# Performance work log

Measured on AMD Instinct MI355X. Metric: run time of the kernel, lower is better.

## Reference

```python
import jax, jax.numpy as jnp
import numpy as np

EPS = 1e-5   # BatchNorm eps (eval mode, running_mean=0, running_var=1 as at init)
NEG = 0.2    # LeakyReLU negative slope


def _conv(W, x):
    # 1x1 conv == channel matmul. W: [out_c, in_c], x: [B, in_c, ...]
    return jnp.einsum('oc,bc...->bo...', W, x)


def _bn(x, g, b):
    # eval-mode BN with running_mean=0, running_var=1
    sh = (1, -1) + (1,) * (x.ndim - 2)
    return x * (g.reshape(sh) / np.float32(np.sqrt(1.0 + EPS))) + b.reshape(sh)


def _lrelu(x):
    return jax.nn.leaky_relu(x, NEG)


def _knn_idx(pos, k):
    # pos: [B, 3, N] -> idx [B, N, k] of k nearest points (incl. self)
    sq = jnp.sum(pos * pos, axis=1)                      # [B, N]
    inner = jnp.einsum('bcn,bcm->bnm', pos, pos)         # [B, N, N]
    dist = sq[:, :, None] + sq[:, None, :] - 2.0 * inner
    _, idx = jax.lax.top_k(-dist, k)
    return idx


def _gather(points, idx):
    # points [B, N, C], idx [B, N, K] -> [B, N, K, C]
    return jax.vmap(lambda p, i: p[i])(points, idx)


def setup_inputs() -> dict:
    key = jax.random.key(0)
    B, N, K = 2, 8192, 16
    d_points, d_model = 64, 64
    ks = jax.random.split(key, 24)
    w = lambda k_, o, i: (jax.random.normal(k_, (o, i), jnp.float32) * 0.05)
    gm = lambda k_, c: (1.0 + 0.1 * jax.random.normal(k_, (c,), jnp.float32))
    bt = lambda k_, c: (0.1 * jax.random.normal(k_, (c,), jnp.float32))
    return {
        'feats': jax.random.normal(ks[0], (B, d_points, N), jnp.float32),
        'pos': jax.random.uniform(ks[1], (B, 3, N), jnp.float32),
        'k': K,
        'W1': w(ks[2], d_model, d_points), 'g1': gm(ks[3], d_model), 'b1': bt(ks[4], d_model),
        'Wq': w(ks[5], d_model, d_model), 'Wk': w(ks[6], d_model, d_model), 'Wv': w(ks[7], d_model, d_model),
        'Wd1': w(ks[8], d_model, 3), 'gd1': gm(ks[9], d_model), 'bd1': bt(ks[10], d_model),
        'Wd2': w(ks[11], d_model, d_model), 'gd2': gm(ks[12], d_model), 'bd2': bt(ks[13], d_model),
        'Wg1': w(ks[14], d_model, d_model), 'gg1': gm(ks[15], d_model), 'bg1': bt(ks[16], d_model),
        'Wg2': w(ks[17], d_model, d_model), 'gg2': gm(ks[18], d_model), 'bg2': bt(ks[19], d_model),
        'W2': w(ks[20], d_points, d_model), 'g2': gm(ks[21], d_points), 'b2': bt(ks[22], d_points),
    }


def reference(feats, pos, k, W1, g1, b1, Wq, Wk, Wv,
              Wd1, gd1, bd1, Wd2, gd2, bd2,
              Wg1, gg1, bg1, Wg2, gg2, bg2, W2, g2, b2):
    B, _, N = feats.shape
    knn_idx = _knn_idx(pos, k)                            # [B, N, K]
    pos_nc = jnp.transpose(pos, (0, 2, 1))                # [B, N, 3]
    knn_pos = _gather(pos_nc, knn_idx)                    # [B, N, K, 3]

    x = _lrelu(_bn(_conv(W1, feats), g1, b1))             # [B, d, N]
    q = _conv(Wq, x)                                      # [B, d, N]
    k_feat = _gather(jnp.transpose(_conv(Wk, x), (0, 2, 1)), knn_idx)
    k_t = jnp.transpose(k_feat, (0, 3, 2, 1))             # [B, d, K, N]
    v_feat = _gather(jnp.transpose(_conv(Wv, x), (0, 2, 1)), knn_idx)
    v_t = jnp.transpose(v_feat, (0, 3, 2, 1))             # [B, d, K, N]

    rel = pos_nc[:, :, None, :] - knn_pos                 # [B, N, K, 3]
    rel_t = jnp.transpose(rel, (0, 3, 2, 1))              # [B, 3, K, N]
    pe = _lrelu(_bn(_conv(Wd1, rel_t), gd1, bd1))
    pos_enc = _lrelu(_bn(_conv(Wd2, pe), gd2, bd2))       # [B, d, K, N]

    a = q[:, :, None, :] - k_t + pos_enc                  # [B, d, K, N]
    a = _lrelu(_bn(_conv(Wg1, a), gg1, bg1))
    a = _lrelu(_bn(_conv(Wg2, a), gg2, bg2))
    # torch: attn / sqrt(k.size(-1)) where k has shape [B, d, K, N] -> sqrt(N)
    attn = jax.nn.softmax(a / jnp.sqrt(jnp.float32(N)), axis=-2)

    res = jnp.einsum('bmnf,bmnf->bmf', attn, v_t + pos_enc)  # [B, d, N]
    out = _lrelu(_bn(_conv(W2, res), g2, b2)) + feats
    return out
```

## Files before the change

kernel.cpp:

```cpp
#include <hip/hip_runtime.h>
#include <hip/hip_bf16.h>
#include <math.h>

namespace {

constexpr int B = 2;
constexpr int N = 8192;
constexpr int D = 64;
constexpr int GRID = 10;
constexpr int GC = GRID * GRID * GRID;
constexpr float H = 0.1f;
constexpr float NEGS = 0.2f;
constexpr float BN_INV = 0.9999950000374997f;
constexpr float RSQN = 0.011048543456039806f;
constexpr int KNN_BLOCKS = B * N / 16;

typedef __attribute__((ext_vector_type(8))) short bf16x8;
typedef __attribute__((ext_vector_type(16))) float f32x16;

union Frag { int4 i4; unsigned u[4]; bf16x8 h; };

__device__ __forceinline__ float lrelu(float v) { return fmaxf(v, NEGS * v); }

__device__ __forceinline__ unsigned pk2(float a, float b) {
  __hip_bfloat162 h2 = __float22bfloat162_rn(make_float2(a, b));
  unsigned r;
  __builtin_memcpy(&r, &h2, 4);
  return r;
}
__device__ __forceinline__ float blo(unsigned u) { return __uint_as_float(u << 16); }
__device__ __forceinline__ float bhi(unsigned u) { return __uint_as_float(u & 0xFFFF0000u); }

__device__ __forceinline__ f32x16 MF(int4 a, const Frag& b, f32x16 c) {
  Frag af; af.i4 = a;
  return __builtin_amdgcn_mfma_f32_32x32x16_bf16(af.h, b.h, c, 0, 0, 0);
}

template <int CTRL>
__device__ __forceinline__ float dpp_add(float v) {
  int t = __builtin_amdgcn_update_dpp(0, __float_as_int(v), CTRL, 0xF, 0xF, false);
  return v + __int_as_float(t);
}
__device__ __forceinline__ float rsum16(float v) {
  v = dpp_add<0x128>(v);
  v = dpp_add<0x124>(v);
  v = dpp_add<0x122>(v);
  v = dpp_add<0x121>(v);
  return v;
}
template <int CTRL>
__device__ __forceinline__ unsigned long long dpp_min_u64(unsigned long long k) {
  int lo = __builtin_amdgcn_update_dpp(0, (int)(unsigned)k, CTRL, 0xF, 0xF, false);
  int hi = __builtin_amdgcn_update_dpp(0, (int)(unsigned)(k >> 32), CTRL, 0xF, 0xF, false);
  unsigned long long o = ((unsigned long long)(unsigned)hi << 32) | (unsigned)lo;
  return o < k ? o : k;
}
__device__ __forceinline__ unsigned long long rmin16_u64(unsigned long long k) {
  k = dpp_min_u64<0x128>(k);
  k = dpp_min_u64<0x124>(k);
  k = dpp_min_u64<0x122>(k);
  k = dpp_min_u64<0x121>(k);
  return k;
}

__device__ __forceinline__ int cellco(float v) {
  int c = (int)(v * 10.0f);
  return min(max(c, 0), GRID - 1);
}

__device__ __forceinline__ void buildB(const f32x16& x0, const f32x16& x1, int h, Frag Bf[4]) {
  unsigned Z[8][2];
  #pragma unroll
  for (int q = 0; q < 4; ++q) {
    Z[q][0]     = pk2(x0[4*q+0], x0[4*q+1]);
    Z[q][1]     = pk2(x0[4*q+2], x0[4*q+3]);
    Z[4+q][0]   = pk2(x1[4*q+0], x1[4*q+1]);
    Z[4+q][1]   = pk2(x1[4*q+2], x1[4*q+3]);
  }
  unsigned S[8][2];
  #pragma unroll
  for (int q = 0; q < 8; ++q) {
    S[q][0] = (unsigned)__shfl_xor((int)Z[q][0], 32);
    S[q][1] = (unsigned)__shfl_xor((int)Z[q][1], 32);
  }
  #pragma unroll
  for (int t = 0; t < 4; ++t) {
    int qq = (t >> 1) * 4 + 2 * (t & 1);
    Bf[t].u[0] = h ? S[qq+1][0] : Z[qq][0];
    Bf[t].u[1] = h ? S[qq+1][1] : Z[qq][1];
    Bf[t].u[2] = h ? Z[qq+1][0] : S[qq][0];
    Bf[t].u[3] = h ? Z[qq+1][1] : S[qq][1];
  }
}

__device__ __forceinline__ f32x16 biasAct(f32x16 d, const float4* bp, int mt, int h) {
  f32x16 r;
  #pragma unroll
  for (int q = 0; q < 4; ++q) {
    float4 bb = bp[h * 8 + mt * 4 + q];
    r[4*q+0] = lrelu(d[4*q+0] + bb.x);
    r[4*q+1] = lrelu(d[4*q+1] + bb.y);
    r[4*q+2] = lrelu(d[4*q+2] + bb.z);
    r[4*q+3] = lrelu(d[4*q+3] + bb.w);
  }
  return r;
}

struct PrepArgs {
  const float* W[9];
  const float* scale[9];
  const float* bias[5];
  const float* bd1;
};

__global__ __launch_bounds__(256) void prep_kernel(PrepArgs a, unsigned short* AF, float* biasAll) {
  int mi = blockIdx.x;
  int tid = threadIdx.x;
  if (mi < 8) {
    int off = (mi == 7) ? 29696 : mi * 4096;
    const float* W = a.W[mi];
    const float* G = a.scale[mi];
    unsigned short* dst = AF + off;
    for (int e = tid; e < 4096; e += 256) {
      int i = e & 7, lane = (e >> 3) & 63, t = (e >> 9) & 3, mt = e >> 11;
      int row = 32 * mt + (lane & 31);
      int k = 16 * t + 8 * (lane >> 5) + i;
      float v = W[row * 64 + k];
      if (G) v *= G[row] * BN_INV;
      if (mi == 6) v *= RSQN;
      __hip_bfloat16 hb = __float2bfloat16(v);
      __builtin_memcpy(&dst[e], &hb, 2);
    }
  } else {
    const float* W = a.W[8];
    const float* G = a.scale[8];
    for (int e = tid; e < 1024; e += 256) {
      int i = e & 7, lane = (e >> 3) & 63, mt = e >> 9;
      int row = 32 * mt + (lane & 31), h = lane >> 5;
      float v = 0.f;
      if (h == 0) {
        if (i < 3) v = W[row * 3 + i] * G[row] * BN_INV;
        else if (i == 3) v = a.bd1[row];
      }
      __hip_bfloat16 hb = __float2bfloat16(v);
      __builtin_memcpy(&AF[28672 + e], &hb, 2);
    }
    for (int e = tid; e < 320; e += 256) {
      int ai = e >> 6, idx = e & 63;
      int h = idx >> 5, mt = (idx >> 4) & 1, q = (idx >> 2) & 3, j = idx & 3;
      float bv = a.bias[ai][32 * mt + 8 * q + 4 * h + j];
      if (ai == 3) bv *= RSQN;
      biasAll[e] = bv;
    }
  }
}

__global__ __launch_bounds__(256) void pos4cid_kernel(
    const float* __restrict__ pos, float* __restrict__ pos4,
    int* __restrict__ cid16, int* __restrict__ cellCount)
{
  int i = blockIdx.x * 256 + threadIdx.x;
  int b = i >> 13;
  int n = i & (N - 1);
  const float* pb = pos + (size_t)b * 3 * N;
  float x = pb[n], y = pb[N + n], z = pb[2 * N + n];
  float4 v = {x, y, z, x * x + y * y + z * z};
  *reinterpret_cast<float4*>(pos4 + (size_t)i * 4) = v;
  int cid = (cellco(z) * GRID + cellco(y)) * GRID + cellco(x);
  cid16[i] = cid;
  atomicAdd(&cellCount[b * GC + cid], 1);
}

__global__ __launch_bounds__(1024) void scan_kernel(
    const int* __restrict__ cnt, int* __restrict__ cellStart)
{
  __shared__ int s[2][2048];
  int t = threadIdx.x;
  s[0][t] = cnt[t];
  s[0][t + 1024] = cnt[t + 1024];
  __syncthreads();
  int src = 0;
  for (int off = 1; off < 2048; off <<= 1) {
    int dst = src ^ 1;
    for (int i = t; i < 2048; i += 1024) {
      int v = s[src][i];
      if (i >= off) v += s[src][i - off];
      s[dst][i] = v;
    }
    __syncthreads();
    src ^= 1;
  }
  cellStart[t] = (t == 0) ? 0 : s[src][t - 1];
  cellStart[t + 1024] = s[src][t + 1023];
}

__global__ __launch_bounds__(256) void scatter_kernel(
    const float* __restrict__ pos4, const int* __restrict__ cid16,
    const int* __restrict__ cellStart, int* __restrict__ cellOfs,
    float4* __restrict__ pos4s, int* __restrict__ sid, int* __restrict__ inv)
{
  int i = blockIdx.x * 256 + threadIdx.x;
  int b = i >> 13;
  int cg = b * GC + cid16[i];
  int dst = cellStart[cg] + atomicAdd(&cellOfs[cg], 1);
  pos4s[dst] = *reinterpret_cast<const float4*>(pos4 + (size_t)i * 4);
  sid[dst] = i & (N - 1);
  inv[i] = dst;
}

__global__ __launch_bounds__(256) void knnqkv_kernel(
    const float4* __restrict__ pos4s, const int* __restrict__ sid,
    const int* __restrict__ cellStart, int* __restrict__ knn_s,
    const float* __restrict__ feats, const int4* __restrict__ AF,
    const float* __restrict__ b1p, const int* __restrict__ inv,
    uint2* __restrict__ qT, uint2* __restrict__ kT, uint2* __restrict__ vT)
{
  __shared__ int4 sA[1024];

  if (blockIdx.x < KNN_BLOCKS) {
    constexpr unsigned long long SENT = ~0ULL;
    int lq = threadIdx.x & 15;
    int wid = (blockIdx.x * 256 + threadIdx.x) >> 4;
    int b = wid >> 13;
    float4 q = pos4s[wid];
    int cx = cellco(q.x), cy = cellco(q.y), cz = cellco(q.z);
    const int cbase = b * GC;
    int myout = 0;

    int nb = (int)(cx == 0 || cx == GRID - 1) + (int)(cy == 0 || cy == GRID - 1)
           + (int)(cz == 0 || cz == GRID - 1);
    int r0 = (nb >= 2) ? 2 : 1;

    bool done = false;
    #pragma unroll 1
    for (int r = r0; r < GRID; ++r) {
      if (!done) {
        unsigned long long dk[16];
        #pragma unroll
        for (int j = 0; j < 16; ++j) dk[j] = SENT;

        int x0 = max(cx - r, 0), x1 = min(cx + r, GRID - 1);
        int y0 = max(cy - r, 0), y1 = min(cy + r, GRID - 1);
        int z0 = max(cz - r, 0), z1 = min(cz + r, GRID - 1);
        #pragma unroll 1
        for (int zz = z0; zz <= z1; ++zz) {
          #pragma unroll 1
          for (int yy = y0; yy <= y1; ++yy) {
            int rowc = cbase + (zz * GRID + yy) * GRID;
            int i0 = cellStart[rowc + x0], i1 = cellStart[rowc + x1 + 1];
            #pragma unroll 1
            for (int i = i0 + lq; i < i1; i += 16) {
              float4 cp = pos4s[i];
              float inn = q.x * cp.x + q.y * cp.y + q.z * cp.z;
              float dist = fmaxf(fmaf(-2.f, inn, q.w + cp.w), 0.f);
              unsigned long long key =
                  ((unsigned long long)__float_as_uint(dist) << 26) |
                  ((unsigned long long)(unsigned)sid[i] << 13) |
                  (unsigned long long)(unsigned)(i & (N - 1));
              if (key < dk[15]) {
                bool bj = true;
                #pragma unroll
                for (int j = 15; j >= 1; --j) {
                  bool bjm1 = key < dk[j - 1];
                  dk[j] = bj ? (bjm1 ? dk[j - 1] : key) : dk[j];
                  bj = bjm1;
                }
                if (bj) dk[0] = key;
              }
            }
          }
        }

        float dlast = 0.f;
        #pragma unroll 1
        for (int e = 0; e < 16; ++e) {
          unsigned long long m = rmin16_u64(dk[0]);
          if (dk[0] == m) {
            #pragma unroll
            for (int j = 0; j < 15; ++j) dk[j] = dk[j + 1];
            dk[15] = SENT;
          }
          if (lq == e) myout = (int)(m & 0x1FFFULL);
          dlast = __uint_as_float((unsigned)(m >> 26));
        }

        float mg = 3.4e38f;
        if (cx - r > 0)        mg = fminf(mg, q.x - (cx - r) * H);
        if (cx + r < GRID - 1) mg = fminf(mg, (cx + r + 1) * H - q.x);
        if (cy - r > 0)        mg = fminf(mg, q.y - (cy - r) * H);
        if (cy + r < GRID - 1) mg = fminf(mg, (cy + r + 1) * H - q.y);
        if (cz - r > 0)        mg = fminf(mg, q.z - (cz - r) * H);
        if (cz + r < GRID - 1) mg = fminf(mg, (cz + r + 1) * H - q.z);
        done = (dlast <= mg * mg * 0.999f);
      }
      if (__all(done)) break;
    }

    knn_s[(size_t)wid * 16 + lq] = myout;
    return;
  }

  int qb = blockIdx.x - KNN_BLOCKS;
  int my = qb >> 7;
  int gx = qb & 127;
  for (int i = threadIdx.x; i < 512; i += 256) {
    sA[i] = AF[i];
    sA[512 + i] = AF[512 * (1 + my) + i];
  }
  __syncthreads();
  int lane = threadIdx.x & 63, w = threadIdx.x >> 6;
  int gw = gx * 4 + w;
  int col = lane & 31, h = lane >> 5;
  int nb_ = gw * 32;
  int b = nb_ >> 13;
  int n = (nb_ & (N - 1)) + col;
  size_t gpt = (size_t)b * N + n;
  int sv = inv[gpt];
  const float* fb = feats + (size_t)b * D * N + n;

  Frag Bf[4];
  #pragma unroll
  for (int t = 0; t < 4; ++t) {
    int c0 = 16 * t + 8 * h;
    float f[8];
    #pragma unroll
    for (int i = 0; i < 8; ++i) f[i] = fb[(size_t)(c0 + i) * N];
    #pragma unroll
    for (int d_ = 0; d_ < 4; ++d_) Bf[t].u[d_] = pk2(f[2*d_], f[2*d_+1]);
  }
  f32x16 acc0 = {}, acc1 = {};
  #pragma unroll
  for (int t = 0; t < 4; ++t) {
    acc0 = MF(sA[t * 64 + lane], Bf[t], acc0);
    acc1 = MF(sA[(4 + t) * 64 + lane], Bf[t], acc1);
  }
  const float4* bp = (const float4*)b1p;
  f32x16 x0 = biasAct(acc0, bp, 0, h);
  f32x16 x1 = biasAct(acc1, bp, 1, h);
  Frag Bx[4];
  buildB(x0, x1, h, Bx);

  uint2* op = (my == 0) ? qT : (my == 1) ? kT : vT;
  f32x16 a0 = {}, a1 = {};
  #pragma unroll
  for (int t = 0; t < 4; ++t) {
    a0 = MF(sA[512 + t * 64 + lane], Bx[t], a0);
    a1 = MF(sA[512 + (4 + t) * 64 + lane], Bx[t], a1);
  }
  #pragma unroll
  for (int q = 0; q < 4; ++q) {
    uint2 v0, v1;
    v0.x = pk2(a0[4*q+0], a0[4*q+1]); v0.y = pk2(a0[4*q+2], a0[4*q+3]);
    v1.x = pk2(a1[4*q+0], a1[4*q+1]); v1.y = pk2(a1[4*q+2], a1[4*q+3]);
    op[(size_t)sv * 16 + 2 * q + h] = v0;
    op[(size_t)sv * 16 + 8 + 2 * q + h] = v1;
  }
}

__global__ __launch_bounds__(256) void fused_kernel(
    const float4* __restrict__ pos4s, const int* __restrict__ sid,
    const int* __restrict__ knn_s,
    const uint2* __restrict__ qT, const uint2* __restrict__ kT, const uint2* __restrict__ vT,
    const int4* __restrict__ AF,
    const float* __restrict__ biases,
    uint2* __restrict__ res_ws)
{
  int lane = threadIdx.x & 63, w = threadIdx.x >> 6;
  int gw = blockIdx.x * 4 + w;
  int col = lane & 31, h = lane >> 5;
  int p = col >> 4, kk = col & 15;
  int sbase = gw * 2;
  int b = sbase >> 13;
  int s = sbase + p;

  int m_loc = knn_s[(size_t)s * 16 + kk];
  int orig = sid[s];
  float4 P = pos4s[s];

  __shared__ int4 sA[1664];
  for (int i = threadIdx.x; i < 1664; i += 256) sA[i] = AF[i];
  __syncthreads();
  const float4* bpd2 = (const float4*)(biases);
  const float4* bpg1 = (const float4*)(biases + 64);
  const float4* bpg2 = (const float4*)(biases + 128);

  size_t ms = (size_t)b * N + m_loc;
  float4 Q = pos4s[ms];
  float rx = P.x - Q.x, ry = P.y - Q.y, rz = P.z - Q.z;

  Frag B0;
  B0.u[0] = h ? 0u : pk2(rx, ry);
  B0.u[1] = h ? 0u : pk2(rz, 1.0f);
  B0.u[2] = 0u; B0.u[3] = 0u;
  f32x16 acc0 = {}, acc1 = {};
  acc0 = MF(sA[1536 + lane], B0, acc0);
  acc1 = MF(sA[1600 + lane], B0, acc1);
  f32x16 pe0, pe1;
  #pragma unroll
  for (int i = 0; i < 16; ++i) { pe0[i] = lrelu(acc0[i]); pe1[i] = lrelu(acc1[i]); }
  Frag Bp[4];
  buildB(pe0, pe1, h, Bp);

  acc0 = (f32x16){}; acc1 = (f32x16){};
  #pragma unroll
  for (int t = 0; t < 4; ++t) {
    acc0 = MF(sA[t * 64 + lane], Bp[t], acc0);
    acc1 = MF(sA[(4 + t) * 64 + lane], Bp[t], acc1);
  }
  f32x16 pn0 = biasAct(acc0, bpd2, 0, h);
  f32x16 pn1 = biasAct(acc1, bpd2, 1, h);

  unsigned pep[8][2];
  #pragma unroll
  for (int q = 0; q < 4; ++q) {
    pep[q][0]   = pk2(pn0[4*q+0], pn0[4*q+1]);
    pep[q][1]   = pk2(pn0[4*q+2], pn0[4*q+3]);
    pep[4+q][0] = pk2(pn1[4*q+0], pn1[4*q+1]);
    pep[4+q][1] = pk2(pn1[4*q+2], pn1[4*q+3]);
  }

  f32x16 av0, av1;
  #pragma unroll
  for (int mt = 0; mt < 2; ++mt) {
    f32x16& dst = mt ? av1 : av0;
    const f32x16& pn = mt ? pn1 : pn0;
    #pragma unroll
    for (int q = 0; q < 4; ++q) {
      uint2 qq_ = qT[(size_t)s * 16 + 8 * mt + 2 * q + h];
      uint2 kq_ = kT[ms * 16 + 8 * mt + 2 * q + h];
      dst[4*q+0] = pn[4*q+0] + blo(qq_.x) - blo(kq_.x);
      dst[4*q+1] = pn[4*q+1] + bhi(qq_.x) - bhi(kq_.x);
      dst[4*q+2] = pn[4*q+2] + blo(qq_.y) - blo(kq_.y);
      dst[4*q+3] = pn[4*q+3] + bhi(qq_.y) - bhi(kq_.y);
    }
  }
  buildB(av0, av1, h, Bp);

  acc0 = (f32x16){}; acc1 = (f32x16){};
  #pragma unroll
  for (int t = 0; t < 4; ++t) {
    acc0 = MF(sA[512 + t * 64 + lane], Bp[t], acc0);
    acc1 = MF(sA[512 + (4 + t) * 64 + lane], Bp[t], acc1);
  }
  f32x16 a10 = biasAct(acc0, bpg1, 0, h);
  f32x16 a11 = biasAct(acc1, bpg1, 1, h);
  buildB(a10, a11, h, Bp);

  acc0 = (f32x16){}; acc1 = (f32x16){};
  #pragma unroll
  for (int t = 0; t < 4; ++t) {
    acc0 = MF(sA[1024 + t * 64 + lane], Bp[t], acc0);
    acc1 = MF(sA[1024 + (4 + t) * 64 + lane], Bp[t], acc1);
  }
  f32x16 at0 = biasAct(acc0, bpg2, 0, h);
  f32x16 at1 = biasAct(acc1, bpg2, 1, h);

  uint2* rp = res_ws + ((size_t)b * N + orig) * 16;
  #pragma unroll
  for (int mt = 0; mt < 2; ++mt) {
    const f32x16& at = mt ? at1 : at0;
    f32x16 ev, nm;
    #pragma unroll
    for (int q = 0; q < 4; ++q) {
      uint2 vq_ = vT[ms * 16 + 8 * mt + 2 * q + h];
      unsigned pp0 = pep[mt * 4 + q][0], pp1 = pep[mt * 4 + q][1];
      float vp0 = blo(vq_.x) + blo(pp0);
      float vp1 = bhi(vq_.x) + bhi(pp0);
      float vp2 = blo(vq_.y) + blo(pp1);
      float vp3 = bhi(vq_.y) + bhi(pp1);
      ev[4*q+0] = __expf(at[4*q+0]); nm[4*q+0] = ev[4*q+0] * vp0;
      ev[4*q+1] = __expf(at[4*q+1]); nm[4*q+1] = ev[4*q+1] * vp1;
      ev[4*q+2] = __expf(at[4*q+2]); nm[4*q+2] = ev[4*q+2] * vp2;
      ev[4*q+3] = __expf(at[4*q+3]); nm[4*q+3] = ev[4*q+3] * vp3;
    }
    #pragma unroll
    for (int i = 0; i < 16; ++i) {
      ev[i] = rsum16(ev[i]);
      nm[i] = rsum16(nm[i]);
    }
    if (kk == 0) {
      #pragma unroll
      for (int q = 0; q < 4; ++q) {
        uint2 rr;
        rr.x = pk2(nm[4*q+0] / ev[4*q+0], nm[4*q+1] / ev[4*q+1]);
        rr.y = pk2(nm[4*q+2] / ev[4*q+2], nm[4*q+3] / ev[4*q+3]);
        rp[8 * mt + 2 * q + h] = rr;
      }
    }
  }
}

__global__ __launch_bounds__(256) void final_kernel(
    const uint2* __restrict__ res_ws, const int4* __restrict__ AF,
    const float* __restrict__ b2p, const float* __restrict__ feats,
    float* __restrict__ out)
{
  __shared__ int4 sA[512];
  for (int i = threadIdx.x; i < 512; i += 256) sA[i] = AF[i];
  __syncthreads();
  int lane = threadIdx.x & 63, w = threadIdx.x >> 6;
  int gw = blockIdx.x * 4 + w;
  int col = lane & 31, h = lane >> 5;
  int nb = gw * 32;
  int b = nb >> 13;
  int n = (nb & (N - 1)) + col;
  size_t g = (size_t)b * N + n;
  const int4* rp = (const int4*)(res_ws + (size_t)g * 16);
  Frag Br[4];
  #pragma unroll
  for (int t = 0; t < 4; ++t) Br[t].i4 = rp[2 * t + h];
  f32x16 a0 = {}, a1 = {};
  #pragma unroll
  for (int t = 0; t < 4; ++t) {
    a0 = MF(sA[t * 64 + lane], Br[t], a0);
    a1 = MF(sA[(4 + t) * 64 + lane], Br[t], a1);
  }
  const float4* bp = (const float4*)b2p;
  f32x16 o0 = biasAct(a0, bp, 0, h);
  f32x16 o1 = biasAct(a1, bp, 1, h);
  const float* fb = feats + (size_t)b * D * N;
  float* ob = out + (size_t)b * D * N;
  #pragma unroll
  for (int mt = 0; mt < 2; ++mt) {
    const f32x16& oo = mt ? o1 : o0;
    #pragma unroll
    for (int q = 0; q < 4; ++q) {
      #pragma unroll
      for (int j = 0; j < 4; ++j) {
        int chan = 32 * mt + 8 * q + 4 * h + j;
        ob[(size_t)chan * N + n] = oo[4*q+j] + fb[(size_t)chan * N + n];
      }
    }
  }
}

}

extern "C" void kernel_launch(void* const* d_in, const int* in_sizes, int n_in,
                              void* d_out, int out_size, void* d_ws, size_t ws_size,
                              hipStream_t stream) {
  const float* feats = (const float*)d_in[0];
  const float* pos   = (const float*)d_in[1];
  const float* W1  = (const float*)d_in[3];
  const float* g1  = (const float*)d_in[4];
  const float* b1  = (const float*)d_in[5];
  const float* Wq  = (const float*)d_in[6];
  const float* Wk  = (const float*)d_in[7];
  const float* Wv  = (const float*)d_in[8];
  const float* Wd1 = (const float*)d_in[9];
  const float* gd1 = (const float*)d_in[10];
  const float* bd1 = (const float*)d_in[11];
  const float* Wd2 = (const float*)d_in[12];
  const float* gd2 = (const float*)d_in[13];
  const float* bd2 = (const float*)d_in[14];
  const float* Wg1 = (const float*)d_in[15];
  const float* gg1 = (const float*)d_in[16];
  const float* bg1 = (const float*)d_in[17];
  const float* Wg2 = (const float*)d_in[18];
  const float* gg2 = (const float*)d_in[19];
  const float* bg2 = (const float*)d_in[20];
  const float* W2  = (const float*)d_in[21];
  const float* g2  = (const float*)d_in[22];
  const float* b2  = (const float*)d_in[23];

  uint8_t* wsb = (uint8_t*)d_ws;
  unsigned short* AF = (unsigned short*)wsb;
  float* biasAll = (float*)(wsb + 73728);
  float* pos4    = (float*)(wsb + 75008);
  uint2* qTb     = (uint2*)(wsb + 337152);
  uint2* kTb     = (uint2*)(wsb + 2434304);
  uint2* vTb     = (uint2*)(wsb + 4531456);
  uint2* res_ws  = (uint2*)(wsb + 6628608);
  int*   cid16     = (int*)(wsb + 10822912);
  int*   cellCount = (int*)(wsb + 10888448);
  int*   cellStart = (int*)(wsb + 10896640);
  int*   cellOfs   = (int*)(wsb + 10904832);
  float4* pos4s    = (float4*)(wsb + 10913024);
  int*   sid       = (int*)(wsb + 11175168);
  int*   knn_s     = (int*)(wsb + 11240704);
  int*   inv       = (int*)(wsb + 12289280);

  PrepArgs pa;
  pa.W[0] = W1;  pa.W[1] = Wq;  pa.W[2] = Wk;  pa.W[3] = Wv;
  pa.W[4] = Wd2; pa.W[5] = Wg1; pa.W[6] = Wg2; pa.W[7] = W2; pa.W[8] = Wd1;
  pa.scale[0] = g1;  pa.scale[1] = nullptr; pa.scale[2] = nullptr; pa.scale[3] = nullptr;
  pa.scale[4] = gd2; pa.scale[5] = gg1;     pa.scale[6] = gg2;     pa.scale[7] = g2; pa.scale[8] = gd1;
  pa.bias[0] = b1; pa.bias[1] = bd2; pa.bias[2] = bg1; pa.bias[3] = bg2; pa.bias[4] = b2;
  pa.bd1 = bd1;

  hipMemsetAsync(cellCount, 0, 2048 * sizeof(int), stream);
  hipMemsetAsync(cellOfs, 0, 2048 * sizeof(int), stream);
  hipLaunchKernelGGL(prep_kernel, dim3(9), dim3(256), 0, stream, pa, AF, biasAll);
  hipLaunchKernelGGL(pos4cid_kernel, dim3(B * N / 256), dim3(256), 0, stream,
                     pos, pos4, cid16, cellCount);
  hipLaunchKernelGGL(scan_kernel, dim3(1), dim3(1024), 0, stream, cellCount, cellStart);
  hipLaunchKernelGGL(scatter_kernel, dim3(B * N / 256), dim3(256), 0, stream,
                     pos4, cid16, cellStart, cellOfs, pos4s, sid, inv);
  hipLaunchKernelGGL(knnqkv_kernel, dim3(KNN_BLOCKS + 384), dim3(256), 0, stream,
                     pos4s, sid, cellStart, knn_s,
                     feats, (const int4*)wsb, biasAll, inv, qTb, kTb, vTb);
  hipLaunchKernelGGL(fused_kernel, dim3(B * N / 8), dim3(256), 0, stream,
                     pos4s, sid, knn_s, qTb, kTb, vTb,
                     (const int4*)(wsb + 32768), biasAll + 64, res_ws);
  hipLaunchKernelGGL(final_kernel, dim3(128), dim3(256), 0, stream,
                     res_ws, (const int4*)(wsb + 59392), biasAll + 256, feats, (float*)d_out);
}
```

Before: 144.6 us.

## Scan only the new shell in grid kNN and defer the top-k merge

Per-lane top-16 lists now persist across search radii, so each expansion scans only the newly added shell of cells instead of rescanning the whole cube. The termination test counts candidates under the distance threshold with a 16-lane sum, replacing the per-radius 16-step cross-lane min merge, which now runs once after the loop. This removes redundant distance evaluations and merge passes for points that need more than one radius, at the cost of more branching and segmented row scans.

New measurement: 128.2 us. 1.13x faster.

```diff
diff --git a/kernel.cpp b/kernel.cpp
--- a/kernel.cpp
+++ b/kernel.cpp
@@ -225,64 +225,65 @@
     float4 q = pos4s[wid];
     int cx = cellco(q.x), cy = cellco(q.y), cz = cellco(q.z);
     const int cbase = b * GC;
-    int myout = 0;
 
     int nb = (int)(cx == 0 || cx == GRID - 1) + (int)(cy == 0 || cy == GRID - 1)
            + (int)(cz == 0 || cz == GRID - 1);
     int r0 = (nb >= 2) ? 2 : 1;
 
-    bool done = false;
+    unsigned long long dk[16];
+    #pragma unroll
+    for (int j = 0; j < 16; ++j) dk[j] = SENT;
+
+    auto scanSeg = [&](int i0, int i1) {
+      #pragma unroll 1
+      for (int i = i0 + lq; i < i1; i += 16) {
+        float4 cp = pos4s[i];
+        float inn = q.x * cp.x + q.y * cp.y + q.z * cp.z;
+        float dist = fmaxf(fmaf(-2.f, inn, q.w + cp.w), 0.f);
+        unsigned long long key =
+            ((unsigned long long)__float_as_uint(dist) << 26) |
+            ((unsigned long long)(unsigned)sid[i] << 13) |
+            (unsigned long long)(unsigned)(i & (N - 1));
+        if (key < dk[15]) {
+          bool bj = true;
+          #pragma unroll
+          for (int j = 15; j >= 1; --j) {
+            bool bjm1 = key < dk[j - 1];
+            dk[j] = bj ? (bjm1 ? dk[j - 1] : key) : dk[j];
+            bj = bjm1;
+          }
+          if (bj) dk[0] = key;
+        }
+      }
+    };
+
+    bool done = false, first = true;
     #pragma unroll 1
-    for (int r = r0; r < GRID; ++r) {
-      if (!done) {
-        unsigned long long dk[16];
-        #pragma unroll
-        for (int j = 0; j < 16; ++j) dk[j] = SENT;
-
+    for (int r = 1; r < GRID; ++r) {
+      if (r >= r0 && !done) {
         int x0 = max(cx - r, 0), x1 = min(cx + r, GRID - 1);
         int y0 = max(cy - r, 0), y1 = min(cy + r, GRID - 1);
         int z0 = max(cz - r, 0), z1 = min(cz + r, GRID - 1);
+        int rin = first ? -1 : r - 1;
+        int xi0 = max(cx - rin, 0), xi1 = min(cx + rin, GRID - 1);
+        int yi0 = max(cy - rin, 0), yi1 = min(cy + rin, GRID - 1);
+        int zi0 = max(cz - rin, 0), zi1 = min(cz + rin, GRID - 1);
         #pragma unroll 1
         for (int zz = z0; zz <= z1; ++zz) {
+          bool zout = (zz < zi0) || (zz > zi1);
           #pragma unroll 1
           for (int yy = y0; yy <= y1; ++yy) {
+            bool rowfull = zout || (yy < yi0) || (yy > yi1);
             int rowc = cbase + (zz * GRID + yy) * GRID;
-            int i0 = cellStart[rowc + x0], i1 = cellStart[rowc + x1 + 1];
-            #pragma unroll 1
-            for (int i = i0 + lq; i < i1; i += 16) {
-              float4 cp = pos4s[i];
-              float inn = q.x * cp.x + q.y * cp.y + q.z * cp.z;
-              float dist = fmaxf(fmaf(-2.f, inn, q.w + cp.w), 0.f);
-              unsigned long long key =
-                  ((unsigned long long)__float_as_uint(dist) << 26) |
-                  ((unsigned long long)(unsigned)sid[i] << 13) |
-                  (unsigned long long)(unsigned)(i & (N - 1));
-              if (key < dk[15]) {
-                bool bj = true;
-                #pragma unroll
-                for (int j = 15; j >= 1; --j) {
-                  bool bjm1 = key < dk[j - 1];
-                  dk[j] = bj ? (bjm1 ? dk[j - 1] : key) : dk[j];
-                  bj = bjm1;
-                }
-                if (bj) dk[0] = key;
-              }
+            if (rowfull) {
+              scanSeg(cellStart[rowc + x0], cellStart[rowc + x1 + 1]);
+            } else {
+              if (x0 < xi0) scanSeg(cellStart[rowc + x0], cellStart[rowc + xi0]);
+              if (xi1 < x1) scanSeg(cellStart[rowc + xi1 + 1], cellStart[rowc + x1 + 1]);
             }
           }
         }
-
-        float dlast = 0.f;
-        #pragma unroll 1
-        for (int e = 0; e < 16; ++e) {
-          unsigned long long m = rmin16_u64(dk[0]);
-          if (dk[0] == m) {
-            #pragma unroll
-            for (int j = 0; j < 15; ++j) dk[j] = dk[j + 1];
-            dk[15] = SENT;
-          }
-          if (lq == e) myout = (int)(m & 0x1FFFULL);
-          dlast = __uint_as_float((unsigned)(m >> 26));
-        }
+        first = false;
 
         float mg = 3.4e38f;
         if (cx - r > 0)        mg = fminf(mg, q.x - (cx - r) * H);
@@ -291,11 +292,28 @@
         if (cy + r < GRID - 1) mg = fminf(mg, (cy + r + 1) * H - q.y);
         if (cz - r > 0)        mg = fminf(mg, q.z - (cz - r) * H);
         if (cz + r < GRID - 1) mg = fminf(mg, (cz + r + 1) * H - q.z);
-        done = (dlast <= mg * mg * 0.999f);
+        float thr = mg * mg * 0.999f;
+        unsigned long long tk = ((unsigned long long)__float_as_uint(thr)) << 26;
+        float c = 0.f;
+        #pragma unroll
+        for (int j = 0; j < 16; ++j) c += (dk[j] < tk) ? 1.f : 0.f;
+        c = rsum16(c);
+        done = (c > 15.5f);
       }
       if (__all(done)) break;
     }
 
+    int myout = 0;
+    #pragma unroll 1
+    for (int e = 0; e < 16; ++e) {
+      unsigned long long m = rmin16_u64(dk[0]);
+      if (dk[0] == m) {
+        #pragma unroll
+        for (int j = 0; j < 15; ++j) dk[j] = dk[j + 1];
+        dk[15] = SENT;
+      }
+      if (lq == e) myout = (int)(m & 0x1FFFULL);
+    }
     knn_s[(size_t)wid * 16 + lq] = myout;
     return;
   }
```
